# Performance work log

Measured on AMD Instinct MI355X. Metric: run time of the kernel, lower is better.

Reference implementation:

```python
import jax, jax.numpy as jnp
import numpy as np

B, T, A, F, K, DQ, DV = 64, 1024, 128, 1024, 31, 1024, 512  # filters F == T required by source math


def setup_inputs() -> dict:
    key = jax.random.key(0)
    ks = jax.random.split(key, 8)
    s = 0.05
    return {
        "query": jax.random.normal(ks[0], (B, 1, DQ), jnp.float32),
        "value": jax.random.normal(ks[1], (B, T, DV), jnp.float32),
        "attention_weights_cat": jax.random.uniform(ks[2], (B, T, 2), jnp.float32),
        "Wq": jax.random.normal(ks[3], (DQ, A), jnp.float32) * s,
        "Wm": jax.random.normal(ks[4], (DV, A), jnp.float32) * s,
        "Wv": jax.random.normal(ks[5], (A, 1), jnp.float32) * s,
        "Wconv": jax.random.normal(ks[6], (K, 2, F), jnp.float32) * s,
        "Wloc": jax.random.normal(ks[7], (T, A), jnp.float32) * s,
    }


def reference(query, value, attention_weights_cat, Wq, Wm, Wv, Wconv, Wloc):
    # query_layer: Dense(tanh, no bias): [B,1,DQ] -> [B,1,A]
    q = jnp.tanh(jnp.einsum('bld,da->bla', query, Wq))
    # memory_layer: Dense(tanh, no bias): [B,T,DV] -> [B,T,A]
    v = jnp.tanh(jnp.einsum('btd,da->bta', value, Wm))
    # location conv (SAME, no bias): [B,T,2] -> [B,T,F]
    loc = jax.lax.conv_general_dilated(
        attention_weights_cat, Wconv, window_strides=(1,), padding='SAME',
        dimension_numbers=('NWC', 'WIO', 'NWC'))
    # source transposes [0,2,1] then Dense(T->A, tanh): [B,F,T] -> [B,F,A]
    loc = jnp.tanh(jnp.einsum('bft,ta->bfa', jnp.transpose(loc, (0, 2, 1)), Wloc))
    # additive score (F == T so broadcast add is element-aligned): [B,T,1]
    score = jnp.einsum('bta,ao->bto', jnp.tanh(q + v + loc), Wv)
    alignment = jax.nn.softmax(score, axis=1)                # softmax over time
    context = jnp.sum(alignment * v, axis=1)                  # [B,A]
    return context, jnp.transpose(alignment, (0, 2, 1))       # [B,1,T]
```

## Files before the change

kernel.cpp:

```cpp
#include <hip/hip_runtime.h>
#include <hip/hip_bf16.h>

#define BB 64
#define TT 1024
#define AA 128
#define FF 1024
#define DQ 1024
#define DV 512

typedef __bf16 bf16x8_t __attribute__((ext_vector_type(8)));
typedef __bf16 bf16x4_t __attribute__((ext_vector_type(4)));
typedef float f32x4_t __attribute__((ext_vector_type(4)));
typedef _Float16 f16x4_t __attribute__((ext_vector_type(4)));

__device__ __forceinline__ float ftanh(float x) {
    float e = __expf(2.0f * x);
    return 1.0f - 2.0f / (e + 1.0f);
}

__device__ __forceinline__ __bf16 bhi(float x) { return (__bf16)x; }
__device__ __forceinline__ __bf16 blo(float x) {
    __bf16 h = (__bf16)x;
    return (__bf16)(x - (float)h);
}

__global__ __launch_bounds__(256) void k_prep(
    const float* __restrict__ Wm, const float* __restrict__ Wconv,
    const float* __restrict__ Wloc, const float* __restrict__ query,
    const float* __restrict__ Wq,
    __bf16* __restrict__ pwmhi, __bf16* __restrict__ pwmlo,
    __bf16* __restrict__ wcthi, __bf16* __restrict__ wctlo,
    __bf16* __restrict__ pwlhi, __bf16* __restrict__ pwllo,
    float* __restrict__ q_ws) {
    __shared__ float ls[128 * 65];
    int bx = blockIdx.x, tid = threadIdx.x;
    if (bx < 16) {
        int s = bx, d0 = s * 32;
        for (int i = tid; i < 4096; i += 256) {
            int dd = i >> 7, a = i & 127;
            ls[a * 33 + dd] = Wm[(d0 + dd) * AA + a];
        }
        __syncthreads();
#pragma unroll
        for (int u = 0; u < 2; u++) {
            int pos = tid * 2 + u;
            int l15 = pos & 15, lq = (pos >> 4) & 3, g = pos >> 6;
            bf16x8_t h8, l8;
#pragma unroll
            for (int j = 0; j < 8; j++) {
                float x = ls[(g * 16 + l15) * 33 + lq * 8 + j];
                h8[j] = bhi(x);
                l8[j] = blo(x);
            }
            size_t off = (size_t)(s * 512 + pos) * 8;
            *(bf16x8_t*)(pwmhi + off) = h8;
            *(bf16x8_t*)(pwmlo + off) = l8;
        }
    } else if (bx < 24) {
        int f0 = (bx - 16) * 128;
        for (int i = tid; i < 8192; i += 256) {
            int kc = i >> 7, f = i & 127;
            ls[f * 65 + kc] = (kc < 62) ? Wconv[kc * FF + f0 + f] : 0.f;
        }
        __syncthreads();
        int f = tid >> 1, half = tid & 1;
#pragma unroll
        for (int g = 0; g < 4; g++) {
            bf16x8_t h8, l8;
#pragma unroll
            for (int j = 0; j < 8; j++) {
                float x = ls[f * 65 + half * 32 + g * 8 + j];
                h8[j] = bhi(x);
                l8[j] = blo(x);
            }
            size_t off = (size_t)(f0 + f) * 64 + half * 32 + g * 8;
            *(bf16x8_t*)(wcthi + off) = h8;
            *(bf16x8_t*)(wctlo + off) = l8;
        }
    } else if (bx < 56) {
        int s2 = bx - 24, t0 = s2 * 32;
        for (int i = tid; i < 4096; i += 256) {
            int tt = i >> 7, a = i & 127;
            ls[a * 33 + tt] = Wloc[(t0 + tt) * AA + a];
        }
        __syncthreads();
#pragma unroll
        for (int u = 0; u < 2; u++) {
            int pos = tid * 2 + u;
            int l15 = pos & 15, lq = (pos >> 4) & 3, g = pos >> 6;
            bf16x8_t h8, l8;
#pragma unroll
            for (int j = 0; j < 8; j++) {
                float x = ls[(g * 16 + l15) * 33 + lq * 8 + j];
                h8[j] = bhi(x);
                l8[j] = blo(x);
            }
            size_t off = (size_t)(s2 * 512 + pos) * 8;
            *(bf16x8_t*)(pwlhi + off) = h8;
            *(bf16x8_t*)(pwllo + off) = l8;
        }
    } else {
        int b = bx - 56;
        int a = tid & 127, half = tid >> 7;
        const float* qrow = query + b * DQ + half * 512;
        float a0 = 0.f, a1 = 0.f, a2 = 0.f, a3 = 0.f;
        for (int d = 0; d < 512; d += 4) {
            float4 qv = *(const float4*)(qrow + d);
            int dg = (half * 512 + d) * AA + a;
            a0 += qv.x * Wq[dg];
            a1 += qv.y * Wq[dg + AA];
            a2 += qv.z * Wq[dg + 2 * AA];
            a3 += qv.w * Wq[dg + 3 * AA];
        }
        ls[tid] = a0 + a1 + a2 + a3;
        __syncthreads();
        if (half == 0) q_ws[b * AA + a] = ftanh(ls[a] + ls[a + 128]);
    }
}

__global__ __launch_bounds__(256) void k_zq(
    const float* __restrict__ xcat,
    const __bf16* __restrict__ pwlhi, const __bf16* __restrict__ pwllo,
    __bf16* __restrict__ zthi, __bf16* __restrict__ ztlo) {
    int bx = blockIdx.x;
    int b = bx & 63, ah = bx >> 6;
    int tid = threadIdx.x;
    __shared__ float xs0[1056], xs1[1056];
    __shared__ float zs[64 * 66];
    for (int i = tid; i < 1056; i += 256) {
        int t = i - 16;
        float2 xv = (t >= 0 && t < TT) ? *(const float2*)(xcat + (size_t)(b * TT + t) * 2)
                                       : make_float2(0.f, 0.f);
        xs0[i] = xv.x;
        xs1[i] = xv.y;
    }
    __syncthreads();
    int lane = tid & 63, wid = tid >> 6;
    int wm = wid >> 1, wn = wid & 1;
    int l15 = lane & 15, lq = lane >> 4;

    f32x4_t zacc[2][2];
#pragma unroll
    for (int mi = 0; mi < 2; mi++)
#pragma unroll
        for (int ni = 0; ni < 2; ni++) zacc[mi][ni] = (f32x4_t){0.f, 0.f, 0.f, 0.f};

    int phase = bx & 31;
    for (int sl = 0; sl < 32; sl++) {
        int s = (sl + phase) & 31;
        int t0 = s * 32;
        bf16x8_t bh[2], bl[2];
#pragma unroll
        for (int ni = 0; ni < 2; ni++) {
            int g = ah * 4 + wn * 2 + ni;
            size_t poff = (size_t)((s * 8 + g) * 64 + lane) * 8;
            bh[ni] = *(const bf16x8_t*)(pwlhi + poff);
            bl[ni] = *(const bf16x8_t*)(pwllo + poff);
        }
        bf16x8_t ah_[2], al_[2];
#pragma unroll
        for (int mi = 0; mi < 2; mi++) {
            int kc = wm * 32 + mi * 16 + l15;
            const float* xsc = (kc & 1) ? xs1 : xs0;
            int base = t0 + lq * 8 + (kc >> 1) + 1;
#pragma unroll
            for (int j = 0; j < 8; j++) {
                float x = xsc[base + j];
                ah_[mi][j] = bhi(x);
                al_[mi][j] = blo(x);
            }
        }
#pragma unroll
        for (int ni = 0; ni < 2; ni++)
#pragma unroll
            for (int mi = 0; mi < 2; mi++) {
                zacc[mi][ni] = __builtin_amdgcn_mfma_f32_16x16x32_bf16(ah_[mi], bh[ni], zacc[mi][ni], 0, 0, 0);
                zacc[mi][ni] = __builtin_amdgcn_mfma_f32_16x16x32_bf16(al_[mi], bh[ni], zacc[mi][ni], 0, 0, 0);
                zacc[mi][ni] = __builtin_amdgcn_mfma_f32_16x16x32_bf16(ah_[mi], bl[ni], zacc[mi][ni], 0, 0, 0);
            }
    }
#pragma unroll
    for (int mi = 0; mi < 2; mi++)
#pragma unroll
        for (int ni = 0; ni < 2; ni++)
#pragma unroll
            for (int r = 0; r < 4; r++)
                zs[(wm * 32 + mi * 16 + lq * 4 + r) * 66 + wn * 32 + ni * 16 + l15] = zacc[mi][ni][r];
    __syncthreads();
    int a_local = tid & 63, seg = tid >> 6;
#pragma unroll
    for (int g = 0; g < 2; g++) {
        bf16x8_t h8, l8;
#pragma unroll
        for (int j = 0; j < 8; j++) {
            float x = zs[(seg * 16 + g * 8 + j) * 66 + a_local];
            h8[j] = bhi(x);
            l8[j] = blo(x);
        }
        size_t off = ((size_t)b * AA + ah * 64 + a_local) * 64 + seg * 16 + g * 8;
        *(bf16x8_t*)(zthi + off) = h8;
        *(bf16x8_t*)(ztlo + off) = l8;
    }
}

__global__ __launch_bounds__(256, 2) void k_main(
    const float* __restrict__ value,
    const __bf16* __restrict__ pwmhi, const __bf16* __restrict__ pwmlo,
    const __bf16* __restrict__ wcthi, const __bf16* __restrict__ wctlo,
    const __bf16* __restrict__ zthi, const __bf16* __restrict__ ztlo,
    const float* __restrict__ q_ws, const float* __restrict__ Wv,
    _Float16* __restrict__ v_ws, float* __restrict__ score) {
    int b = blockIdx.x >> 3;
    int trow0 = (blockIdx.x & 7) << 7;
    int tid = threadIdx.x;
    int lane = tid & 63, wid = tid >> 6;
    int wm = wid >> 1, wn = wid & 1;
    int l15 = lane & 15, lq = lane >> 4;

    __shared__ __align__(16) float As[2][128 * 32];
    __shared__ __align__(16) __bf16 Bh[2][512 * 8];
    __shared__ __align__(16) __bf16 Bl[2][512 * 8];
    __shared__ float sc_red[256];

    f32x4_t acc[4][4];
#pragma unroll
    for (int mi = 0; mi < 4; mi++)
#pragma unroll
        for (int ni = 0; ni < 4; ni++) acc[mi][ni] = (f32x4_t){0.f, 0.f, 0.f, 0.f};

    int l3 = lane >> 3;
    int su = (lane & 7) ^ l3;
    const float* aG[4];
    unsigned aL[4];
#pragma unroll
    for (int i = 0; i < 4; i++) {
        int row = (wid * 4 + i) * 8 + l3;
        aG[i] = value + (size_t)(b * TT + trow0 + row) * DV + su * 4;
        aL[i] = (unsigned)((wid * 4 + i) * 1024);
    }
    const __bf16* bGh[2];
    const __bf16* bGl[2];
    unsigned bL[2];
#pragma unroll
    for (int j = 0; j < 2; j++) {
        int c = (wid * 2 + j) * 64 + lane;
        bGh[j] = pwmhi + (size_t)c * 8;
        bGl[j] = pwmlo + (size_t)c * 8;
        bL[j] = (unsigned)((wid * 2 + j) * 1024);
    }

#define STAGE(bf, s)                                                                        \
    {                                                                                       \
        _Pragma("unroll") for (int i = 0; i < 4; i++)                                       \
            __builtin_amdgcn_global_load_lds(                                               \
                (const __attribute__((address_space(1))) void*)(aG[i] + (s) * 32),          \
                (__attribute__((address_space(3))) void*)((char*)&As[bf][0] + aL[i]),       \
                16, 0, 0);                                                                  \
        _Pragma("unroll") for (int j = 0; j < 2; j++) {                                     \
            __builtin_amdgcn_global_load_lds(                                               \
                (const __attribute__((address_space(1))) void*)(bGh[j] + (size_t)(s) * 4096),\
                (__attribute__((address_space(3))) void*)((char*)&Bh[bf][0] + bL[j]),       \
                16, 0, 0);                                                                  \
            __builtin_amdgcn_global_load_lds(                                               \
                (const __attribute__((address_space(1))) void*)(bGl[j] + (size_t)(s) * 4096),\
                (__attribute__((address_space(3))) void*)((char*)&Bl[bf][0] + bL[j]),       \
                16, 0, 0);                                                                  \
        }                                                                                   \
    }

    STAGE(0, 0);
    __syncthreads();

    int swz = l15 & 7;
    for (int it = 0; it < 16; ++it) {
        int cb = it & 1;
        if (it < 15) STAGE(cb ^ 1, it + 1);

        bf16x8_t ah[4], al[4];
#pragma unroll
        for (int mi = 0; mi < 4; mi++) {
            int row = wm * 64 + mi * 16 + l15;
            const char* rbase = (const char*)&As[cb][0] + row * 128;
            f32x4_t f0 = *(const f32x4_t*)(rbase + (((lq * 2 + 0) ^ swz) << 4));
            f32x4_t f1 = *(const f32x4_t*)(rbase + (((lq * 2 + 1) ^ swz) << 4));
#pragma unroll
            for (int j = 0; j < 4; j++) {
                ah[mi][j] = bhi(f0[j]);
                al[mi][j] = blo(f0[j]);
                ah[mi][4 + j] = bhi(f1[j]);
                al[mi][4 + j] = blo(f1[j]);
            }
        }
        bf16x8_t bh[4], bl[4];
#pragma unroll
        for (int ni = 0; ni < 4; ni++) {
            int c = (wn * 4 + ni) * 64 + lane;
            bh[ni] = *(const bf16x8_t*)(&Bh[cb][0] + (size_t)c * 8);
            bl[ni] = *(const bf16x8_t*)(&Bl[cb][0] + (size_t)c * 8);
        }
#pragma unroll
        for (int mi = 0; mi < 4; mi++)
#pragma unroll
            for (int ni = 0; ni < 4; ni++) {
                acc[mi][ni] = __builtin_amdgcn_mfma_f32_16x16x32_bf16(ah[mi], bh[ni], acc[mi][ni], 0, 0, 0);
                acc[mi][ni] = __builtin_amdgcn_mfma_f32_16x16x32_bf16(al[mi], bh[ni], acc[mi][ni], 0, 0, 0);
                acc[mi][ni] = __builtin_amdgcn_mfma_f32_16x16x32_bf16(ah[mi], bl[ni], acc[mi][ni], 0, 0, 0);
            }
        __syncthreads();
    }
#undef STAGE

    f32x4_t lacc[4][4];
#pragma unroll
    for (int mi = 0; mi < 4; mi++)
#pragma unroll
        for (int ni = 0; ni < 4; ni++) lacc[mi][ni] = (f32x4_t){0.f, 0.f, 0.f, 0.f};
#pragma unroll
    for (int kc0 = 0; kc0 < 64; kc0 += 32) {
        bf16x8_t a2h[4], a2l[4], b2h[4], b2l[4];
#pragma unroll
        for (int mi = 0; mi < 4; mi++) {
            int f = trow0 + wm * 64 + mi * 16 + l15;
            a2h[mi] = *(const bf16x8_t*)(wcthi + (size_t)f * 64 + kc0 + lq * 8);
            a2l[mi] = *(const bf16x8_t*)(wctlo + (size_t)f * 64 + kc0 + lq * 8);
        }
#pragma unroll
        for (int ni = 0; ni < 4; ni++) {
            int a = wn * 64 + ni * 16 + l15;
            size_t off = ((size_t)b * AA + a) * 64 + kc0 + lq * 8;
            b2h[ni] = *(const bf16x8_t*)(zthi + off);
            b2l[ni] = *(const bf16x8_t*)(ztlo + off);
        }
#pragma unroll
        for (int mi = 0; mi < 4; mi++)
#pragma unroll
            for (int ni = 0; ni < 4; ni++) {
                lacc[mi][ni] = __builtin_amdgcn_mfma_f32_16x16x32_bf16(a2h[mi], b2h[ni], lacc[mi][ni], 0, 0, 0);
                lacc[mi][ni] = __builtin_amdgcn_mfma_f32_16x16x32_bf16(a2l[mi], b2h[ni], lacc[mi][ni], 0, 0, 0);
                lacc[mi][ni] = __builtin_amdgcn_mfma_f32_16x16x32_bf16(a2h[mi], b2l[ni], lacc[mi][ni], 0, 0, 0);
            }
    }

    float qv[4], wv[4];
#pragma unroll
    for (int ni = 0; ni < 4; ni++) {
        int a = wn * 64 + ni * 16 + l15;
        qv[ni] = q_ws[b * AA + a];
        wv[ni] = Wv[a];
    }
#pragma unroll
    for (int mi = 0; mi < 4; mi++) {
#pragma unroll
        for (int r = 0; r < 4; r++) {
            int tl = wm * 64 + mi * 16 + lq * 4 + r;
            int t = trow0 + tl;
            float s = 0.f;
#pragma unroll
            for (int ni = 0; ni < 4; ni++) {
                float v = ftanh(acc[mi][ni][r]);
                float loc = ftanh(lacc[mi][ni][r]);
                int a = wn * 64 + ni * 16 + l15;
                v_ws[(size_t)(b * TT + t) * AA + a] = (_Float16)v;
                s += ftanh(qv[ni] + v + loc) * wv[ni];
            }
            s += __shfl_xor(s, 1, 64);
            s += __shfl_xor(s, 2, 64);
            s += __shfl_xor(s, 4, 64);
            s += __shfl_xor(s, 8, 64);
            if (l15 == 0) sc_red[wn * 128 + tl] = s;
        }
    }
    __syncthreads();
    if (tid < 128) score[b * TT + trow0 + tid] = sc_red[tid] + sc_red[128 + tid];
}

__global__ void k_softmax(const float* __restrict__ score, float* __restrict__ out_align) {
    int b = blockIdx.x, tid = threadIdx.x;
    __shared__ float red[4];
    float s[4];
#pragma unroll
    for (int i = 0; i < 4; i++) s[i] = score[b * TT + tid + i * 256];
    float m = fmaxf(fmaxf(s[0], s[1]), fmaxf(s[2], s[3]));
    for (int off = 32; off; off >>= 1) m = fmaxf(m, __shfl_xor(m, off, 64));
    int wid = tid >> 6;
    if ((tid & 63) == 0) red[wid] = m;
    __syncthreads();
    float M = fmaxf(fmaxf(red[0], red[1]), fmaxf(red[2], red[3]));
    __syncthreads();
    float e[4];
    float sum = 0.f;
#pragma unroll
    for (int i = 0; i < 4; i++) { e[i] = __expf(s[i] - M); sum += e[i]; }
    for (int off = 32; off; off >>= 1) sum += __shfl_xor(sum, off, 64);
    if ((tid & 63) == 0) red[wid] = sum;
    __syncthreads();
    float inv = 1.0f / (red[0] + red[1] + red[2] + red[3]);
#pragma unroll
    for (int i = 0; i < 4; i++) out_align[b * TT + tid + i * 256] = e[i] * inv;
}

__global__ void k_context(const float* __restrict__ align, const _Float16* __restrict__ v_ws,
                          float* __restrict__ out_ctx) {
    int b = blockIdx.y, t0 = blockIdx.x * 64, tid = threadIdx.x;
    int a0 = (tid & 31) * 4, tl = tid >> 5;
    __shared__ float sh[8 * 132];
    f32x4_t acc = (f32x4_t){0.f, 0.f, 0.f, 0.f};
    for (int tt = tl; tt < 64; tt += 8) {
        float w = align[b * TT + t0 + tt];
        f16x4_t vv = *(const f16x4_t*)(v_ws + (size_t)(b * TT + t0 + tt) * AA + a0);
        acc[0] += w * (float)vv[0];
        acc[1] += w * (float)vv[1];
        acc[2] += w * (float)vv[2];
        acc[3] += w * (float)vv[3];
    }
    *(f32x4_t*)&sh[tl * 132 + a0] = acc;
    __syncthreads();
    if (tid < 128) {
        float s = 0.f;
#pragma unroll
        for (int j = 0; j < 8; j++) s += sh[j * 132 + tid];
        atomicAdd(out_ctx + b * AA + tid, s);
    }
}

extern "C" void kernel_launch(void* const* d_in, const int* in_sizes, int n_in,
                              void* d_out, int out_size, void* d_ws, size_t ws_size,
                              hipStream_t stream) {
    const float* query = (const float*)d_in[0];
    const float* value = (const float*)d_in[1];
    const float* xcat  = (const float*)d_in[2];
    const float* Wq    = (const float*)d_in[3];
    const float* Wm    = (const float*)d_in[4];
    const float* Wv    = (const float*)d_in[5];
    const float* Wconv = (const float*)d_in[6];
    const float* Wloc  = (const float*)d_in[7];
    float* out = (float*)d_out;

    float* ws = (float*)d_ws;
    float* q_ws  = ws;
    float* sc_ws = q_ws + 8192;
    _Float16* v_ws = (_Float16*)(sc_ws + 65536);
    __bf16* pwmhi = (__bf16*)(sc_ws + 65536 + 4194304);
    __bf16* pwmlo = pwmhi + 65536;
    __bf16* wcthi = pwmlo + 65536;
    __bf16* wctlo = wcthi + 65536;
    __bf16* pwlhi = wctlo + 65536;
    __bf16* pwllo = pwlhi + 131072;
    __bf16* zthi  = pwllo + 131072;
    __bf16* ztlo  = zthi + 524288;

    (void)hipMemsetAsync(out, 0, (size_t)8192 * 4, stream);

    k_prep<<<120, 256, 0, stream>>>(Wm, Wconv, Wloc, query, Wq,
                                    pwmhi, pwmlo, wcthi, wctlo, pwlhi, pwllo, q_ws);
    k_zq<<<128, 256, 0, stream>>>(xcat, pwlhi, pwllo, zthi, ztlo);
    k_main<<<512, 256, 0, stream>>>(value, pwmhi, pwmlo, wcthi, wctlo, zthi, ztlo,
                                    q_ws, Wv, v_ws, sc_ws);
    k_softmax<<<BB, 256, 0, stream>>>(sc_ws, out + 8192);
    k_context<<<dim3(16, BB), 256, 0, stream>>>(out + 8192, v_ws, out);
}
```

Baseline: 268.4 us.

## Load Wm operands directly to registers, split k_zq reduction, drop memset

k_main no longer stages the pre-split Wm hi/lo operands through LDS. Each wave now loads them straight into a double-buffered register set with inline global_load_dwordx4, and blocks start at a staggered k-phase. Freeing that LDS allows launch bounds of 3 blocks per SM. k_zq is split over two K halves into 256 blocks writing fp32 partials, which k_main sums and converts to hi/lo bf16. The output memset is folded into k_softmax. The risks are higher register pressure from the register double buffer, and the inline asm loads may not be tracked correctly by compiler waitcnts.

```diff
diff --git a/kernel.cpp b/kernel.cpp
--- a/kernel.cpp
+++ b/kernel.cpp
@@ -121,9 +121,9 @@
 __global__ __launch_bounds__(256) void k_zq(
     const float* __restrict__ xcat,
     const __bf16* __restrict__ pwlhi, const __bf16* __restrict__ pwllo,
-    __bf16* __restrict__ zthi, __bf16* __restrict__ ztlo) {
+    float* __restrict__ ztf) {
     int bx = blockIdx.x;
-    int b = bx & 63, ah = bx >> 6;
+    int b = bx & 63, ahh = (bx >> 6) & 1, kh = bx >> 7;
     int tid = threadIdx.x;
     __shared__ float xs0[1056], xs1[1056];
     __shared__ float zs[64 * 66];
@@ -145,14 +145,14 @@
 #pragma unroll
         for (int ni = 0; ni < 2; ni++) zacc[mi][ni] = (f32x4_t){0.f, 0.f, 0.f, 0.f};
 
-    int phase = bx & 31;
-    for (int sl = 0; sl < 32; sl++) {
-        int s = (sl + phase) & 31;
+    int phase = bx & 15;
+    for (int sl = 0; sl < 16; sl++) {
+        int s = kh * 16 + ((sl + phase) & 15);
         int t0 = s * 32;
         bf16x8_t bh[2], bl[2];
 #pragma unroll
         for (int ni = 0; ni < 2; ni++) {
-            int g = ah * 4 + wn * 2 + ni;
+            int g = ahh * 4 + wn * 2 + ni;
             size_t poff = (size_t)((s * 8 + g) * 64 + lane) * 8;
             bh[ni] = *(const bf16x8_t*)(pwlhi + poff);
             bl[ni] = *(const bf16x8_t*)(pwllo + poff);
@@ -190,24 +190,24 @@
     int a_local = tid & 63, seg = tid >> 6;
 #pragma unroll
     for (int g = 0; g < 2; g++) {
-        bf16x8_t h8, l8;
-#pragma unroll
-        for (int j = 0; j < 8; j++) {
-            float x = zs[(seg * 16 + g * 8 + j) * 66 + a_local];
-            h8[j] = bhi(x);
-            l8[j] = blo(x);
-        }
-        size_t off = ((size_t)b * AA + ah * 64 + a_local) * 64 + seg * 16 + g * 8;
-        *(bf16x8_t*)(zthi + off) = h8;
-        *(bf16x8_t*)(ztlo + off) = l8;
-    }
-}
-
-__global__ __launch_bounds__(256, 2) void k_main(
+        f32x4_t v0, v1;
+#pragma unroll
+        for (int j = 0; j < 4; j++) {
+            v0[j] = zs[(seg * 16 + g * 8 + j) * 66 + a_local];
+            v1[j] = zs[(seg * 16 + g * 8 + 4 + j) * 66 + a_local];
+        }
+        float* dst = ztf + (size_t)kh * 524288 +
+                     ((size_t)b * AA + ahh * 64 + a_local) * 64 + seg * 16 + g * 8;
+        *(f32x4_t*)dst = v0;
+        *(f32x4_t*)(dst + 4) = v1;
+    }
+}
+
+__global__ __launch_bounds__(256, 3) void k_main(
     const float* __restrict__ value,
     const __bf16* __restrict__ pwmhi, const __bf16* __restrict__ pwmlo,
     const __bf16* __restrict__ wcthi, const __bf16* __restrict__ wctlo,
-    const __bf16* __restrict__ zthi, const __bf16* __restrict__ ztlo,
+    const float* __restrict__ ztf,
     const float* __restrict__ q_ws, const float* __restrict__ Wv,
     _Float16* __restrict__ v_ws, float* __restrict__ score) {
     int b = blockIdx.x >> 3;
@@ -216,10 +216,9 @@
     int lane = tid & 63, wid = tid >> 6;
     int wm = wid >> 1, wn = wid & 1;
     int l15 = lane & 15, lq = lane >> 4;
+    int phase = (blockIdx.x + (blockIdx.x >> 3)) & 15;
 
     __shared__ __align__(16) float As[2][128 * 32];
-    __shared__ __align__(16) __bf16 Bh[2][512 * 8];
-    __shared__ __align__(16) __bf16 Bl[2][512 * 8];
     __shared__ float sc_red[256];
 
     f32x4_t acc[4][4];
@@ -238,43 +237,45 @@
         aG[i] = value + (size_t)(b * TT + trow0 + row) * DV + su * 4;
         aL[i] = (unsigned)((wid * 4 + i) * 1024);
     }
-    const __bf16* bGh[2];
-    const __bf16* bGl[2];
-    unsigned bL[2];
-#pragma unroll
-    for (int j = 0; j < 2; j++) {
-        int c = (wid * 2 + j) * 64 + lane;
-        bGh[j] = pwmhi + (size_t)c * 8;
-        bGl[j] = pwmlo + (size_t)c * 8;
-        bL[j] = (unsigned)((wid * 2 + j) * 1024);
-    }
-
-#define STAGE(bf, s)                                                                        \
+    const __bf16* pbh0 = pwmhi + (size_t)(wn * 256 + lane) * 8;
+    const __bf16* pbl0 = pwmlo + (size_t)(wn * 256 + lane) * 8;
+
+    bf16x8_t bhb[2][4], blb[2][4];
+
+#define GL4(dst, ptr, OFF) \
+    asm volatile("global_load_dwordx4 %0, %1, off offset:" OFF : "=v"(dst) : "v"(ptr))
+#define ISSUE_B(bf, s) { \
+    const __bf16* _bh = pbh0 + (size_t)(s) * 4096; \
+    const __bf16* _bl = pbl0 + (size_t)(s) * 4096; \
+    GL4(bhb[bf][0], _bh, "0"); \
+    GL4(bhb[bf][1], _bh, "1024"); \
+    GL4(bhb[bf][2], _bh, "2048"); \
+    GL4(bhb[bf][3], _bh, "3072"); \
+    GL4(blb[bf][0], _bl, "0"); \
+    GL4(blb[bf][1], _bl, "1024"); \
+    GL4(blb[bf][2], _bl, "2048"); \
+    GL4(blb[bf][3], _bl, "3072"); }
+#define STAGE_A(bf, s)                                                                      \
     {                                                                                       \
         _Pragma("unroll") for (int i = 0; i < 4; i++)                                       \
             __builtin_amdgcn_global_load_lds(                                               \
                 (const __attribute__((address_space(1))) void*)(aG[i] + (s) * 32),          \
                 (__attribute__((address_space(3))) void*)((char*)&As[bf][0] + aL[i]),       \
                 16, 0, 0);                                                                  \
-        _Pragma("unroll") for (int j = 0; j < 2; j++) {                                     \
-            __builtin_amdgcn_global_load_lds(                                               \
-                (const __attribute__((address_space(1))) void*)(bGh[j] + (size_t)(s) * 4096),\
-                (__attribute__((address_space(3))) void*)((char*)&Bh[bf][0] + bL[j]),       \
-                16, 0, 0);                                                                  \
-            __builtin_amdgcn_global_load_lds(                                               \
-                (const __attribute__((address_space(1))) void*)(bGl[j] + (size_t)(s) * 4096),\
-                (__attribute__((address_space(3))) void*)((char*)&Bl[bf][0] + bL[j]),       \
-                16, 0, 0);                                                                  \
-        }                                                                                   \
-    }
-
-    STAGE(0, 0);
-    __syncthreads();
+    }
+
+    {
+        int s0 = phase & 15;
+        ISSUE_B(0, s0);
+        STAGE_A(0, s0);
+    }
 
     int swz = l15 & 7;
+#pragma unroll
     for (int it = 0; it < 16; ++it) {
-        int cb = it & 1;
-        if (it < 15) STAGE(cb ^ 1, it + 1);
+        const int cb = it & 1;
+        __syncthreads();
+        __builtin_amdgcn_sched_barrier(0);
 
         bf16x8_t ah[4], al[4];
 #pragma unroll
@@ -291,24 +292,23 @@
                 al[mi][4 + j] = blo(f1[j]);
             }
         }
-        bf16x8_t bh[4], bl[4];
-#pragma unroll
-        for (int ni = 0; ni < 4; ni++) {
-            int c = (wn * 4 + ni) * 64 + lane;
-            bh[ni] = *(const bf16x8_t*)(&Bh[cb][0] + (size_t)c * 8);
-            bl[ni] = *(const bf16x8_t*)(&Bl[cb][0] + (size_t)c * 8);
+        if (it < 15) {
+            const int s = (it + 1 + phase) & 15;
+            ISSUE_B(cb ^ 1, s);
+            STAGE_A(cb ^ 1, s);
         }
 #pragma unroll
         for (int mi = 0; mi < 4; mi++)
 #pragma unroll
             for (int ni = 0; ni < 4; ni++) {
-                acc[mi][ni] = __builtin_amdgcn_mfma_f32_16x16x32_bf16(ah[mi], bh[ni], acc[mi][ni], 0, 0, 0);
-                acc[mi][ni] = __builtin_amdgcn_mfma_f32_16x16x32_bf16(al[mi], bh[ni], acc[mi][ni], 0, 0, 0);
-                acc[mi][ni] = __builtin_amdgcn_mfma_f32_16x16x32_bf16(ah[mi], bl[ni], acc[mi][ni], 0, 0, 0);
-            }
-        __syncthreads();
-    }
-#undef STAGE
+                acc[mi][ni] = __builtin_amdgcn_mfma_f32_16x16x32_bf16(ah[mi], bhb[cb][ni], acc[mi][ni], 0, 0, 0);
+                acc[mi][ni] = __builtin_amdgcn_mfma_f32_16x16x32_bf16(al[mi], bhb[cb][ni], acc[mi][ni], 0, 0, 0);
+                acc[mi][ni] = __builtin_amdgcn_mfma_f32_16x16x32_bf16(ah[mi], blb[cb][ni], acc[mi][ni], 0, 0, 0);
+            }
+    }
+#undef ISSUE_B
+#undef STAGE_A
+#undef GL4
 
     f32x4_t lacc[4][4];
 #pragma unroll
@@ -327,9 +327,16 @@
 #pragma unroll
         for (int ni = 0; ni < 4; ni++) {
             int a = wn * 64 + ni * 16 + l15;
-            size_t off = ((size_t)b * AA + a) * 64 + kc0 + lq * 8;
-            b2h[ni] = *(const bf16x8_t*)(zthi + off);
-            b2l[ni] = *(const bf16x8_t*)(ztlo + off);
+            const float* zp = ztf + ((size_t)b * AA + a) * 64 + kc0 + lq * 8;
+            f32x4_t z0 = *(const f32x4_t*)zp + *(const f32x4_t*)(zp + 524288);
+            f32x4_t z1 = *(const f32x4_t*)(zp + 4) + *(const f32x4_t*)(zp + 524292);
+#pragma unroll
+            for (int j = 0; j < 4; j++) {
+                b2h[ni][j] = bhi(z0[j]);
+                b2l[ni][j] = blo(z0[j]);
+                b2h[ni][4 + j] = bhi(z1[j]);
+                b2l[ni][4 + j] = blo(z1[j]);
+            }
         }
 #pragma unroll
         for (int mi = 0; mi < 4; mi++)
@@ -374,8 +381,10 @@
     if (tid < 128) score[b * TT + trow0 + tid] = sc_red[tid] + sc_red[128 + tid];
 }
 
-__global__ void k_softmax(const float* __restrict__ score, float* __restrict__ out_align) {
+__global__ void k_softmax(const float* __restrict__ score, float* __restrict__ out_align,
+                          float* __restrict__ out_ctx) {
     int b = blockIdx.x, tid = threadIdx.x;
+    if (tid < 128) out_ctx[b * AA + tid] = 0.f;
     __shared__ float red[4];
     float s[4];
 #pragma unroll
@@ -446,16 +455,13 @@
     __bf16* wctlo = wcthi + 65536;
     __bf16* pwlhi = wctlo + 65536;
     __bf16* pwllo = pwlhi + 131072;
-    __bf16* zthi  = pwllo + 131072;
-    __bf16* ztlo  = zthi + 524288;
-
-    (void)hipMemsetAsync(out, 0, (size_t)8192 * 4, stream);
+    float* ztf = (float*)(pwllo + 131072);
 
     k_prep<<<120, 256, 0, stream>>>(Wm, Wconv, Wloc, query, Wq,
                                     pwmhi, pwmlo, wcthi, wctlo, pwlhi, pwllo, q_ws);
-    k_zq<<<128, 256, 0, stream>>>(xcat, pwlhi, pwllo, zthi, ztlo);
-    k_main<<<512, 256, 0, stream>>>(value, pwmhi, pwmlo, wcthi, wctlo, zthi, ztlo,
+    k_zq<<<256, 256, 0, stream>>>(xcat, pwlhi, pwllo, ztf);
+    k_main<<<512, 256, 0, stream>>>(value, pwmhi, pwmlo, wcthi, wctlo, ztf,
                                     q_ws, Wv, v_ws, sc_ws);
-    k_softmax<<<BB, 256, 0, stream>>>(sc_ws, out + 8192);
+    k_softmax<<<BB, 256, 0, stream>>>(sc_ws, out + 8192, out);
     k_context<<<dim3(16, BB), 256, 0, stream>>>(out + 8192, v_ws, out);
 }
```

Result: slower. 279.6 us (+4.2%).
